# Kernel optimization log

Hardware: AMD Instinct MI355X
Metric: run time of the kernel (lower is better)

Reference implementation:

```python
import jax, jax.numpy as jnp
import numpy as np

B, S, D = 2, 2048, 2048
H = 16
KV_RANK = 512
NOPE, ROPE = 128, 64
QK_HD = NOPE + ROPE  # 192
V_HD = 128
SCALE = QK_HD ** -0.5
EPS = 1.1920929e-07  # torch RMSNorm default eps = finfo(fp32).eps
NEG = -1e9


def rmsnorm(x, w):
    return x * jax.lax.rsqrt(jnp.mean(x * x, axis=-1, keepdims=True) + EPS) * w


def apply_rope(x, freqs):
    # x: (b, s, h, r) interleaved pairs; freqs: (s, r//2) angles
    sh = x.shape
    xr = x.reshape(*sh[:-1], -1, 2)
    a, b = xr[..., 0], xr[..., 1]
    cos = jnp.cos(freqs)[None, :, None, :]
    sin = jnp.sin(freqs)[None, :, None, :]
    return jnp.stack([a * cos - b * sin, a * sin + b * cos], axis=-1).reshape(sh)


def setup_inputs() -> dict:
    key = jax.random.key(0)
    ks = jax.random.split(key, 8)
    inv = lambda k, shape, fan_in: jax.random.uniform(k, shape, jnp.float32, -1.0, 1.0) / np.sqrt(fan_in)
    x = jax.random.normal(ks[0], (B, S, D), jnp.float32)
    freqs = jax.random.uniform(ks[1], (S, ROPE // 2), jnp.float32) * np.float32(np.pi)
    mask = jnp.where(jnp.triu(jnp.ones((S, S), bool), k=1), jnp.float32(NEG), jnp.float32(0.0))
    wq_w = inv(ks[2], (H * QK_HD, D), D)
    wq_b = jnp.zeros((H * QK_HD,), jnp.float32)
    wkv_a_w = inv(ks[3], (KV_RANK + ROPE, D), D)
    wkv_a_b = jnp.zeros((KV_RANK + ROPE,), jnp.float32)
    kv_norm_w = jnp.ones((KV_RANK,), jnp.float32)
    wkv_b_w = inv(ks[4], (H * (NOPE + V_HD), KV_RANK), KV_RANK)
    wo_w = inv(ks[5], (D, H * V_HD), H * V_HD)
    wo_b = jnp.zeros((D,), jnp.float32)
    return dict(x=x, freqs=freqs, mask=mask, wq_w=wq_w, wq_b=wq_b,
                wkv_a_w=wkv_a_w, wkv_a_b=wkv_a_b, kv_norm_w=kv_norm_w,
                wkv_b_w=wkv_b_w, wo_w=wo_w, wo_b=wo_b)


def reference(x, freqs, mask, wq_w, wq_b, wkv_a_w, wkv_a_b, kv_norm_w, wkv_b_w, wo_w, wo_b):
    b, s, _ = x.shape
    # q projection (q_lora_rank == 0 path)
    q = (x @ wq_w.T + wq_b).reshape(b, s, H, QK_HD)
    q_nope, q_pe = q[..., :NOPE], q[..., NOPE:]
    q_pe = apply_rope(q_pe, freqs)
    # latent kv projection
    kv = x @ wkv_a_w.T + wkv_a_b
    kv, k_pe = kv[..., :KV_RANK], kv[..., KV_RANK:]
    k_pe = apply_rope(k_pe[:, :, None, :], freqs)[:, :, 0, :]  # (b, t, r)
    kv_proj = rmsnorm(kv, kv_norm_w)  # (b, t, c)
    wkv_b = wkv_b_w.reshape(H, NOPE + V_HD, KV_RANK)
    # absorb K-nope projection into q
    q_nope = jnp.einsum('bshd,hdc->bshc', q_nope, wkv_b[:, :NOPE])
    scores = (jnp.einsum('bshc,btc->bsht', q_nope, kv_proj)
              + jnp.einsum('bshr,btr->bsht', q_pe, k_pe)) * SCALE
    scores = scores + mask[None, :, None, :]
    scores = jax.nn.softmax(scores.astype(jnp.float32), axis=-1).astype(x.dtype)
    out = jnp.einsum('bsht,btc->bshc', scores, kv_proj)
    out = jnp.einsum('bshc,hdc->bshd', out, wkv_b[:, -V_HD:])
    return out.reshape(b, s, H * V_HD) @ wo_w.T + wo_b
```

## Files before the change

### kernel.cpp

```cpp
#include <hip/hip_runtime.h>
#include <hip/hip_bf16.h>
#include <math.h>

#define B_ 2
#define S_ 2048
#define H_ 16
#define SCALE_ 0.07216878364870323f
#define SL2_ (0.07216878364870323f * 1.4426950408889634f)
#define EPS_ 1.1920929e-07f
#define M0_ 8.0f

typedef __attribute__((ext_vector_type(8))) short bf16x8;
typedef __attribute__((ext_vector_type(4))) float f32x4;
union U4 { uint4 u; bf16x8 v; f32x4 f; };

__device__ __forceinline__ uint bfbits(float x) {
    uint u = __float_as_uint(x);
    return (u + 0x7fffu + ((u >> 16) & 1u)) >> 16;
}
__device__ __forceinline__ uint pack2bf(float a, float b) {
    return bfbits(a) | (bfbits(b) << 16);
}
__device__ __forceinline__ uint cvtpk(float a, float b) {
    uint r;
    asm("v_cvt_pk_bf16_f32 %0, %1, %2" : "=v"(r) : "v"(a), "v"(b));
    return r;
}
__device__ __forceinline__ void gld_lds16(const ushort* g, ushort* l) {
    __builtin_amdgcn_global_load_lds(
        (const __attribute__((address_space(1))) uint*)g,
        (__attribute__((address_space(3))) uint*)l, 16, 0, 0);
}

template<bool OUT_BF16>
__global__ __launch_bounds__(256) void mgemm(
    const ushort* __restrict__ A, int lda, long long aOff1, long long aOff2,
    const ushort* __restrict__ Bm, int ldb, long long bOff1, long long bOff2,
    const float* __restrict__ bias, float scale,
    void* __restrict__ Cv, int ldc, long long cOff1, long long cOff2,
    int K, int zDiv)
{
    __shared__ ushort As[128 * 32];
    __shared__ ushort Bs[128 * 32];

    const int z = blockIdx.z;
    const int z1 = z % zDiv, z2 = z / zDiv;
    A  += z1 * aOff1 + z2 * aOff2;
    Bm += z1 * bOff1 + z2 * bOff2;
    const long long cBase = z1 * cOff1 + z2 * cOff2;

    const int n0 = blockIdx.x * 128;
    const int m0 = blockIdx.y * 128;
    const int tid = threadIdx.x;
    const int w   = tid >> 6;
    const int l   = tid & 63;
    const int m   = l & 15;
    const int q4  = l >> 4;
    const int mw  = (w & 1) * 64;
    const int nw  = (w >> 1) * 64;
    const int sr  = l >> 2;
    const int sc  = l & 3;

    f32x4 acc[4][4];
#pragma unroll
    for (int i = 0; i < 4; ++i)
#pragma unroll
        for (int j = 0; j < 4; ++j) acc[i][j] = (f32x4){0.f, 0.f, 0.f, 0.f};

    for (int k0 = 0; k0 < K; k0 += 32) {
#pragma unroll
        for (int jj = 0; jj < 2; ++jj) {
            const int slot = w * 2 + jj;
            const int row  = slot * 16 + sr;
            const int g    = sc ^ ((row >> 1) & 3);
            gld_lds16(&A[(long long)(m0 + row) * lda + k0 + g * 8], &As[slot * 512]);
            gld_lds16(&Bm[(long long)(n0 + row) * ldb + k0 + g * 8], &Bs[slot * 512]);
        }
        __syncthreads();

        U4 af[4], bf[4];
#pragma unroll
        for (int i = 0; i < 4; ++i) {
            const int ra = mw + i * 16 + m;
            af[i].u = *(const uint4*)&As[ra * 32 + (q4 ^ ((ra >> 1) & 3)) * 8];
            const int rb = nw + i * 16 + m;
            bf[i].u = *(const uint4*)&Bs[rb * 32 + (q4 ^ ((rb >> 1) & 3)) * 8];
        }
#pragma unroll
        for (int i = 0; i < 4; ++i)
#pragma unroll
            for (int j = 0; j < 4; ++j)
                acc[i][j] = __builtin_amdgcn_mfma_f32_16x16x32_bf16(
                    af[i].v, bf[j].v, acc[i][j], 0, 0, 0);
        __syncthreads();
    }

#pragma unroll
    for (int j = 0; j < 4; ++j) {
        const int cn = n0 + nw + j * 16 + m;
        const float bv = bias ? bias[cn] : 0.0f;
#pragma unroll
        for (int i = 0; i < 4; ++i) {
            const int rw = m0 + mw + i * 16 + q4 * 4;
#pragma unroll
            for (int r = 0; r < 4; ++r) {
                const float val = acc[i][j][r] * scale + bv;
                if (OUT_BF16)
                    ((ushort*)Cv)[cBase + (long long)(rw + r) * ldc + cn] =
                        (ushort)bfbits(val);
                else
                    ((float*)Cv)[cBase + (long long)(rw + r) * ldc + cn] = val;
            }
        }
    }
}

__global__ __launch_bounds__(256) void conv_all(
    const float* __restrict__ x, const float* __restrict__ wq,
    const float* __restrict__ wkva, const float* __restrict__ wo,
    const float* __restrict__ wkvb,
    ushort* __restrict__ x_bf, ushort* __restrict__ wq_bf,
    ushort* __restrict__ wkva_bf, ushort* __restrict__ wo_bf,
    ushort* __restrict__ wkvbK, ushort* __restrict__ wkvbV)
{
    const int bid = blockIdx.x;
    const int tid = threadIdx.x;
    if (bid < 8192) {
        const long long i = ((long long)bid * 256 + tid) * 4;
        float4 v = *(const float4*)&x[i];
        uint2 p; p.x = pack2bf(v.x, v.y); p.y = pack2bf(v.z, v.w);
        *(uint2*)&x_bf[i] = p;
    } else if (bid < 14336) {
        const long long i = ((long long)(bid - 8192) * 256 + tid) * 4;
        float4 v = *(const float4*)&wq[i];
        uint2 p; p.x = pack2bf(v.x, v.y); p.y = pack2bf(v.z, v.w);
        *(uint2*)&wq_bf[i] = p;
    } else if (bid < 15616) {
        const int i = ((bid - 14336) * 256 + tid) * 4;
        const int r = i >> 11;
        uint2 p = make_uint2(0u, 0u);
        if (r < 576) {
            float4 v = *(const float4*)&wkva[i];
            p.x = pack2bf(v.x, v.y); p.y = pack2bf(v.z, v.w);
        }
        *(uint2*)&wkva_bf[i] = p;
    } else if (bid < 19712) {
        const long long i = ((long long)(bid - 15616) * 256 + tid) * 4;
        float4 v = *(const float4*)&wo[i];
        uint2 p; p.x = pack2bf(v.x, v.y); p.y = pack2bf(v.z, v.w);
        *(uint2*)&wo_bf[i] = p;
    } else if (bid < 20736) {
        const int i = ((bid - 19712) * 256 + tid) * 4;
        const int h = i >> 16, rem = i & 65535;
        float4 v = *(const float4*)&wkvb[((long long)(h * 256)) * 512 + rem];
        uint2 p; p.x = pack2bf(v.x, v.y); p.y = pack2bf(v.z, v.w);
        *(uint2*)&wkvbK[i] = p;
    } else {
        const int i = ((bid - 20736) * 256 + tid) * 4;
        const int h = i >> 16, rem = i & 65535;
        float4 v = *(const float4*)&wkvb[((long long)(h * 256 + 128)) * 512 + rem];
        uint2 p; p.x = pack2bf(v.x, v.y); p.y = pack2bf(v.z, v.w);
        *(uint2*)&wkvbV[i] = p;
    }
}

__global__ __launch_bounds__(256) void qprep(
    const float* __restrict__ q_raw, const float* __restrict__ freqs,
    ushort* __restrict__ q192)
{
    const int idx = blockIdx.x * 256 + threadIdx.x;
    const int row = idx / 48;
    const int c4  = idx % 48;
    const int bs = row >> 4, h = row & 15;
    const float* src = q_raw + (long long)bs * 3072 + h * 192;
    if (c4 < 32) {
        const int d = c4 * 4;
        float4 v = *(const float4*)&src[d];
        uint2 p;
        p.x = pack2bf(v.x * SL2_, v.y * SL2_);
        p.y = pack2bf(v.z * SL2_, v.w * SL2_);
        *(uint2*)&q192[(long long)row * 192 + d] = p;
    } else {
        const int j = c4 - 32;
        const int s = bs & 2047;
        const float f0 = freqs[s * 32 + j * 2];
        const float f1 = freqs[s * 32 + j * 2 + 1];
        float c0, s0, c1, s1;
        __sincosf(f0, &s0, &c0);
        __sincosf(f1, &s1, &c1);
        float4 v = *(const float4*)&src[128 + j * 4];
        uint2 p;
        p.x = pack2bf((v.x * c0 - v.y * s0) * SL2_, (v.x * s0 + v.y * c0) * SL2_);
        p.y = pack2bf((v.z * c1 - v.w * s1) * SL2_, (v.z * s1 + v.w * c1) * SL2_);
        *(uint2*)&q192[(long long)row * 192 + 128 + j * 4] = p;
    }
}

__global__ __launch_bounds__(64) void kv_post_kernel(
    const float* __restrict__ kv_raw, const float* __restrict__ bias,
    const float* __restrict__ w, const float* __restrict__ freqs,
    ushort* __restrict__ kv_h)
{
    const int bs = blockIdx.x;
    const int lane = threadIdx.x;
    const float* src = kv_raw + (long long)bs * 640;
    ushort* dst = kv_h + (long long)bs * 576;

    const int c = 4 * lane;
    float4 v0 = *(const float4*)&src[c];
    float4 v1 = *(const float4*)&src[256 + c];
    float4 b0 = *(const float4*)&bias[c];
    float4 b1 = *(const float4*)&bias[256 + c];
    v0.x += b0.x; v0.y += b0.y; v0.z += b0.z; v0.w += b0.w;
    v1.x += b1.x; v1.y += b1.y; v1.z += b1.z; v1.w += b1.w;
    float ss = v0.x * v0.x + v0.y * v0.y + v0.z * v0.z + v0.w * v0.w +
               v1.x * v1.x + v1.y * v1.y + v1.z * v1.z + v1.w * v1.w;
#pragma unroll
    for (int o = 32; o; o >>= 1) ss += __shfl_xor(ss, o, 64);
    const float rs = rsqrtf(ss * (1.0f / 512.0f) + EPS_);

    float4 w0 = *(const float4*)&w[c];
    float4 w1 = *(const float4*)&w[256 + c];
    uint2 p0, p1;
    p0.x = pack2bf(v0.x * rs * w0.x, v0.y * rs * w0.y);
    p0.y = pack2bf(v0.z * rs * w0.z, v0.w * rs * w0.w);
    p1.x = pack2bf(v1.x * rs * w1.x, v1.y * rs * w1.y);
    p1.y = pack2bf(v1.z * rs * w1.z, v1.w * rs * w1.w);
    *(uint2*)&dst[c] = p0;
    *(uint2*)&dst[256 + c] = p1;

    if (lane < 32) {
        const int s = bs & 2047;
        const float f = freqs[s * 32 + lane];
        float cs, sn;
        __sincosf(f, &sn, &cs);
        const float a  = src[512 + 2 * lane]     + bias[512 + 2 * lane];
        const float b2 = src[512 + 2 * lane + 1] + bias[512 + 2 * lane + 1];
        *(uint*)&dst[512 + 2 * lane] = pack2bf(a * cs - b2 * sn, a * sn + b2 * cs);
    }
}

__global__ __launch_bounds__(256) void prep_all(
    const ushort* __restrict__ K_h, const ushort* __restrict__ V_hT,
    const ushort* __restrict__ kv_h,
    uint4* __restrict__ khimg, uint4* __restrict__ vhimg,
    uint4* __restrict__ rimg)
{
    const int bid = blockIdx.x;
    if (bid < 4096) {
        const int g = bid * 256 + threadIdx.x;
        const int lane = g & 63, ck = (g >> 6) & 7, h = (g >> 9) & 15;
        const int tile = (g >> 13) & 63, b = g >> 19;
        const int m = lane & 15, q4 = lane >> 4, f = ck >> 1, s = ck & 1;
        const uint4 v = *(const uint4*)&K_h[
            ((long long)(b * S_ + tile * 32 + s * 16 + m)) * 2048 + h * 128 + f * 32 + q4 * 8];
        khimg[(((long long)(b * 64 + tile) * 16 + h) * 8 + ck) * 64 + lane] = v;
    } else if (bid < 8192) {
        const int g = (bid - 4096) * 256 + threadIdx.x;
        const int lane = g & 63, c = (g >> 6) & 7, h = (g >> 9) & 15;
        const int tile = (g >> 13) & 63, b = g >> 19;
        const int m = lane & 15, q4 = lane >> 4;
        const uint4 v = *(const uint4*)&V_hT[
            ((long long)((b * 16 + h) * 128 + c * 16 + m)) * 2048 + tile * 32 + q4 * 8];
        vhimg[(((long long)(b * 64 + tile) * 16 + h) * 8 + c) * 64 + lane] = v;
    } else {
        const int g = (bid - 8192) * 256 + threadIdx.x;
        const int lane = g & 63, ck = (g >> 6) & 3, tile = (g >> 8) & 63, b = g >> 14;
        const int m = lane & 15, q4 = lane >> 4, f2 = ck >> 1, s = ck & 1;
        const uint4 v = *(const uint4*)&kv_h[
            ((long long)(b * S_ + tile * 32 + s * 16 + m)) * 576 + 512 + f2 * 32 + q4 * 8];
        rimg[((long long)(b * 64 + tile) * 4 + ck) * 64 + lane] = v;
    }
}

__global__ __launch_bounds__(256, 2) void attn_kernel(
    const ushort* __restrict__ q192,
    const uint4*  __restrict__ khimg,
    const uint4*  __restrict__ rimg,
    const uint4*  __restrict__ vhimg,
    float* __restrict__ part_o,
    float* __restrict__ part_l)
{
    __shared__ uint buf[2][20 * 256];

    const int p    = blockIdx.x;
    const int h    = blockIdx.y;
    const int zz   = blockIdx.z;
    const int b    = zz >> 1;
    const int par  = zz & 1;
    const int tid  = threadIdx.x;
    const int wid  = tid >> 6;
    const int lane = tid & 63;
    const int m    = lane & 15;
    const int q4   = lane >> 4;
    const bool odd = q4 & 1;

    auto stage = [&](int bs, int it) {
        const long long tb = (long long)(b * 64 + it);
        const uint4* kb = khimg + ((tb * 16 + h) * 8) * 64;
        const uint4* rb = rimg  + (tb * 4) * 64;
        const uint4* vb = vhimg + ((tb * 16 + h) * 8) * 64;
        ushort* l = (ushort*)&buf[bs][0];
        gld_lds16((const ushort*)(kb + (wid    ) * 64 + lane), l + (wid     ) * 512);
        gld_lds16((const ushort*)(kb + (wid + 4) * 64 + lane), l + (wid +  4) * 512);
        gld_lds16((const ushort*)(rb + (wid    ) * 64 + lane), l + (wid +  8) * 512);
        gld_lds16((const ushort*)(vb + (wid    ) * 64 + lane), l + (wid + 12) * 512);
        gld_lds16((const ushort*)(vb + (wid + 4) * 64 + lane), l + (wid + 16) * 512);
    };

    int cur = 0;
    for (int pass = 0; pass < 2; ++pass) {
        const int chunk = pass ? p : (15 - p);
        const int row0a = chunk * 128 + wid * 16;
        const int row0b = row0a + 64;
        const int sRa   = row0a + m;
        const int sRb   = row0b + m;

        U4 qfa[6], qfb[6];
        {
            const uint4* qpa = (const uint4*)(q192 + ((long long)(b * S_ + sRa) * H_ + h) * 192);
            const uint4* qpb = (const uint4*)(q192 + ((long long)(b * S_ + sRb) * H_ + h) * 192);
#pragma unroll
            for (int f = 0; f < 6; ++f) { qfa[f].u = qpa[f * 4 + q4]; qfb[f].u = qpb[f * 4 + q4]; }
        }

        f32x4 oA[8], oB[8];
#pragma unroll
        for (int c = 0; c < 8; ++c) {
            oA[c] = (f32x4){0.f, 0.f, 0.f, 0.f};
            oB[c] = (f32x4){0.f, 0.f, 0.f, 0.f};
        }
        float lA = 0.0f, lB = 0.0f;

        auto softpack = [&](const f32x4 s0, const f32x4 s1, int t0v, int rw0,
                            float& lac) -> U4 {
            float p00, p01, p02, p03, p10, p11, p12, p13;
            if (t0v + 31 <= rw0) {
                p00 = exp2f(s0[0] - M0_); p01 = exp2f(s0[1] - M0_);
                p02 = exp2f(s0[2] - M0_); p03 = exp2f(s0[3] - M0_);
                p10 = exp2f(s1[0] - M0_); p11 = exp2f(s1[1] - M0_);
                p12 = exp2f(s1[2] - M0_); p13 = exp2f(s1[3] - M0_);
            } else {
                const int sR = rw0 + m;
                const int tb0 = t0v + q4 * 4;
                const int tb1 = tb0 + 16;
                p00 = (tb0 + 0 <= sR) ? exp2f(s0[0] - M0_) : 0.0f;
                p01 = (tb0 + 1 <= sR) ? exp2f(s0[1] - M0_) : 0.0f;
                p02 = (tb0 + 2 <= sR) ? exp2f(s0[2] - M0_) : 0.0f;
                p03 = (tb0 + 3 <= sR) ? exp2f(s0[3] - M0_) : 0.0f;
                p10 = (tb1 + 0 <= sR) ? exp2f(s1[0] - M0_) : 0.0f;
                p11 = (tb1 + 1 <= sR) ? exp2f(s1[1] - M0_) : 0.0f;
                p12 = (tb1 + 2 <= sR) ? exp2f(s1[2] - M0_) : 0.0f;
                p13 = (tb1 + 3 <= sR) ? exp2f(s1[3] - M0_) : 0.0f;
            }
            lac += (p00 + p01) + (p02 + p03) + (p10 + p11) + (p12 + p13);
            uint X0 = cvtpk(p00, p01), X1 = cvtpk(p02, p03);
            uint Y0 = cvtpk(p10, p11), Y1 = cvtpk(p12, p13);
            asm("v_permlane32_swap_b32 %0, %1" : "+v"(X0), "+v"(Y0));
            asm("v_permlane32_swap_b32 %0, %1" : "+v"(X1), "+v"(Y1));
            uint u0 = odd ? X0 : Y0;
            uint u1 = odd ? X1 : Y1;
            uint w0 = (uint)__builtin_amdgcn_ds_swizzle((int)u0, 0x401F);
            uint w1 = (uint)__builtin_amdgcn_ds_swizzle((int)u1, 0x401F);
            U4 bb;
            bb.u.x = odd ? w0 : X0;
            bb.u.y = odd ? w1 : X1;
            bb.u.z = odd ? Y0 : w0;
            bb.u.w = odd ? Y1 : w1;
            return bb;
        };

        const int nT2 = 2 * chunk + 2;
        __syncthreads();
        stage(cur, par);

        for (int v = 0; v < nT2; ++v) {
            const int it = 2 * v + par;
            const int t0 = it * 32;
            __syncthreads();
            if (v + 1 < nT2) stage(cur ^ 1, it + 2);
            __builtin_amdgcn_sched_barrier(0);

            const uint* bb0 = &buf[cur][0];
            const int abase = lane * 4;
            const bool liveB = (t0 <= row0b + 15);
            const bool liveA = (t0 <= row0a + 15);
            const bool twoA  = (t0 < row0a);
            const bool twoB  = (t0 < row0b);

            if (liveB) {
                f32x4 sA0 = (f32x4){0.f,0.f,0.f,0.f}, sA1 = (f32x4){0.f,0.f,0.f,0.f};
                f32x4 sB0 = (f32x4){0.f,0.f,0.f,0.f}, sB1 = (f32x4){0.f,0.f,0.f,0.f};

                if (twoA) {
#pragma unroll
                    for (int f = 0; f < 6; ++f) {
                        const int ck = (f < 4) ? f * 2 : (f - 4) * 2 + 8;
                        U4 a0, a1;
                        a0.u = *(const uint4*)&bb0[ck * 256 + abase];
                        a1.u = *(const uint4*)&bb0[(ck + 1) * 256 + abase];
                        sA0 = __builtin_amdgcn_mfma_f32_16x16x32_bf16(a0.v, qfa[f].v, sA0, 0, 0, 0);
                        sB0 = __builtin_amdgcn_mfma_f32_16x16x32_bf16(a0.v, qfb[f].v, sB0, 0, 0, 0);
                        sA1 = __builtin_amdgcn_mfma_f32_16x16x32_bf16(a1.v, qfa[f].v, sA1, 0, 0, 0);
                        sB1 = __builtin_amdgcn_mfma_f32_16x16x32_bf16(a1.v, qfb[f].v, sB1, 0, 0, 0);
                    }
                } else {
#pragma unroll
                    for (int f = 0; f < 6; ++f) {
                        const int ck = (f < 4) ? f * 2 : (f - 4) * 2 + 8;
                        U4 a0;
                        a0.u = *(const uint4*)&bb0[ck * 256 + abase];
                        if (liveA)
                            sA0 = __builtin_amdgcn_mfma_f32_16x16x32_bf16(a0.v, qfa[f].v, sA0, 0, 0, 0);
                        sB0 = __builtin_amdgcn_mfma_f32_16x16x32_bf16(a0.v, qfb[f].v, sB0, 0, 0, 0);
                        if (twoB) {
                            U4 a1;
                            a1.u = *(const uint4*)&bb0[(ck + 1) * 256 + abase];
                            sB1 = __builtin_amdgcn_mfma_f32_16x16x32_bf16(a1.v, qfb[f].v, sB1, 0, 0, 0);
                        }
                    }
                }

                U4 bbB = softpack(sB0, sB1, t0, row0b, lB);
                if (liveA) {
                    U4 bbA = softpack(sA0, sA1, t0, row0a, lA);
#pragma unroll
                    for (int c = 0; c < 8; ++c) {
                        U4 av; av.u = *(const uint4*)&bb0[(12 + c) * 256 + abase];
                        oB[c] = __builtin_amdgcn_mfma_f32_16x16x32_bf16(av.v, bbB.v, oB[c], 0, 0, 0);
                        oA[c] = __builtin_amdgcn_mfma_f32_16x16x32_bf16(av.v, bbA.v, oA[c], 0, 0, 0);
                    }
                } else {
#pragma unroll
                    for (int c = 0; c < 8; ++c) {
                        U4 av; av.u = *(const uint4*)&bb0[(12 + c) * 256 + abase];
                        oB[c] = __builtin_amdgcn_mfma_f32_16x16x32_bf16(av.v, bbB.v, oB[c], 0, 0, 0);
                    }
                }
            }
            cur ^= 1;
        }

        lA += __shfl_xor(lA, 16, 64);
        lA += __shfl_xor(lA, 32, 64);
        lB += __shfl_xor(lB, 16, 64);
        lB += __shfl_xor(lB, 32, 64);

        const int cid  = (b * 16 + h) * 16 + chunk;
        const int slot = cid * 2 + par;
        float* po = part_o + (long long)slot * 16384;
        const int rA = wid * 16 + m;
        const int rB = rA + 64;
#pragma unroll
        for (int c = 0; c < 8; ++c) {
            *(f32x4*)&po[rA * 128 + c * 16 + q4 * 4] = oA[c];
            *(f32x4*)&po[rB * 128 + c * 16 + q4 * 4] = oB[c];
        }
        if (q4 == 0) {
            part_l[slot * 128 + rA] = lA;
            part_l[slot * 128 + rB] = lB;
        }
    }
}

__global__ __launch_bounds__(256) void combine_kernel(
    const float* __restrict__ part_o, const float* __restrict__ part_l,
    ushort* __restrict__ o_h)
{
    const int idx = blockIdx.x * 256 + threadIdx.x;
    const int d4  = (idx & 31) * 4;
    const int r   = (idx >> 5) & 127;
    const int cid = idx >> 12;
    const int chunk = cid & 15, h = (cid >> 4) & 15, b = cid >> 8;
    const long long s0 = (long long)(cid * 2) * 16384 + r * 128 + d4;
    float4 a = *(const float4*)&part_o[s0];
    float4 c = *(const float4*)&part_o[s0 + 16384];
    const float l = part_l[cid * 256 + r] + part_l[cid * 256 + 128 + r];
    const float inv = 1.0f / l;
    uint2 pk;
    pk.x = cvtpk((a.x + c.x) * inv, (a.y + c.y) * inv);
    pk.y = cvtpk((a.z + c.z) * inv, (a.w + c.w) * inv);
    const int s = chunk * 128 + r;
    *(uint2*)&o_h[(((long long)(b * S_ + s)) * H_ + h) * 128 + d4] = pk;
}

extern "C" void kernel_launch(void* const* d_in, const int* in_sizes, int n_in,
                              void* d_out, int out_size, void* d_ws, size_t ws_size,
                              hipStream_t stream)
{
    const float* x         = (const float*)d_in[0];
    const float* freqs     = (const float*)d_in[1];
    const float* wq_w      = (const float*)d_in[3];
    const float* wq_b      = (const float*)d_in[4];
    const float* wkv_a_w   = (const float*)d_in[5];
    const float* wkv_a_b   = (const float*)d_in[6];
    const float* kv_norm_w = (const float*)d_in[7];
    const float* wkv_b_w   = (const float*)d_in[8];
    const float* wo_w      = (const float*)d_in[9];
    const float* wo_b      = (const float*)d_in[10];
    float* out = (float*)d_out;

    char* w = (char*)d_ws;
    ushort* wo_bf   = (ushort*)w;  w += 8388608;
    uint4*  khimg   = (uint4*)w;   w += 16777216;
    uint4*  vhimg   = (uint4*)w;   w += 16777216;
    uint4*  rimg    = (uint4*)w;   w += 524288;
    ushort* q192    = (ushort*)w;  w += 25165824;
    ushort* o_h     = (ushort*)w;  w += 16777216;
    char* SCR = w;
    ushort* x_bf    = (ushort*)(SCR);
    ushort* wq_bf   = (ushort*)(SCR + 16777216);
    ushort* wkva_bf = (ushort*)(SCR + 29360128);
    ushort* wkvbK   = (ushort*)(SCR + 31981568);
    ushort* wkvbV   = (ushort*)(SCR + 34078720);
    float*  kv_raw  = (float*)(SCR + 36175872);
    float*  q_raw   = (float*)(SCR + 46661632);
    ushort* kv_h    = (ushort*)(SCR);
    ushort* K_h     = (ushort*)(SCR + 4718592);
    ushort* V_hT    = (ushort*)(SCR + 36175872);
    float*  part_o  = (float*)(SCR);
    float*  part_l  = (float*)(SCR + 67108864);

    dim3 blk(256);

    conv_all<<<dim3(21760), blk, 0, stream>>>(
        x, wq_w, wkv_a_w, wo_w, wkv_b_w,
        x_bf, wq_bf, wkva_bf, wo_bf, wkvbK, wkvbV);

    mgemm<false><<<dim3(24, 32, 1), blk, 0, stream>>>(
        x_bf, 2048, 0LL, 0LL, wq_bf, 2048, 0LL, 0LL, wq_b, 1.0f,
        q_raw, 3072, 0LL, 0LL, 2048, 1);

    mgemm<false><<<dim3(5, 32, 1), blk, 0, stream>>>(
        x_bf, 2048, 0LL, 0LL, wkva_bf, 2048, 0LL, 0LL, nullptr, 1.0f,
        kv_raw, 640, 0LL, 0LL, 2048, 1);

    qprep<<<dim3(12288), blk, 0, stream>>>(q_raw, freqs, q192);

    kv_post_kernel<<<dim3(4096), dim3(64), 0, stream>>>(
        kv_raw, wkv_a_b, kv_norm_w, freqs, kv_h);

    mgemm<true><<<dim3(1, 16, 32), blk, 0, stream>>>(
        kv_h, 576, 0LL, (long long)S_ * 576,
        wkvbK, 512, 65536LL, 0LL, nullptr, 1.0f,
        K_h, 2048, 128LL, (long long)S_ * 2048, 512, 16);
    mgemm<true><<<dim3(16, 1, 32), blk, 0, stream>>>(
        wkvbV, 512, 65536LL, 0LL,
        kv_h, 576, 0LL, (long long)S_ * 576, nullptr, 1.0f,
        V_hT, 2048, 262144LL, 4194304LL, 512, 16);

    prep_all<<<dim3(8320), blk, 0, stream>>>(K_h, V_hT, kv_h, khimg, vhimg, rimg);

    attn_kernel<<<dim3(8, 16, 4), blk, 0, stream>>>(
        q192, khimg, rimg, vhimg, part_o, part_l);

    combine_kernel<<<dim3(8192), blk, 0, stream>>>(part_o, part_l, o_h);

    mgemm<false><<<dim3(16, 32, 1), blk, 0, stream>>>(
        o_h, 2048, 0LL, 0LL, wo_bf, 2048, 0LL, 0LL, wo_b, 1.0f,
        out, 2048, 0LL, 0LL, 2048, 1);
}
```

Baseline: 466.0 us.

## Write attention tile images directly from GEMM epilogues and drop prep_all

The K and V projection GEMMs now scatter their bf16 results straight into the tiled khimg/vhimg layouts the attention kernel consumes. kv_post writes the rope part directly into rimg, which removes the separate prep_all repacking kernel and its intermediate K_h/V_hT buffers. The GEMM block index is also remapped so neighbouring blocks spread across groups of 8, aimed at cache or XCD locality. The attention grid is reordered so heads and batch sit in the fastest-varying dimension. The scattered 2-byte epilogue stores may coalesce poorly.

```diff
diff --git a/kernel.cpp b/kernel.cpp
--- a/kernel.cpp
+++ b/kernel.cpp
@@ -32,7 +32,7 @@
         (__attribute__((address_space(3))) uint*)l, 16, 0, 0);
 }
 
-template<bool OUT_BF16>
+template<int OM>
 __global__ __launch_bounds__(256) void mgemm(
     const ushort* __restrict__ A, int lda, long long aOff1, long long aOff2,
     const ushort* __restrict__ Bm, int ldb, long long bOff1, long long bOff2,
@@ -49,8 +49,19 @@
     Bm += z1 * bOff1 + z2 * bOff2;
     const long long cBase = z1 * cOff1 + z2 * cOff2;
 
-    const int n0 = blockIdx.x * 128;
-    const int m0 = blockIdx.y * 128;
+    int bx = blockIdx.x, by = blockIdx.y;
+    {
+        const int gx = gridDim.x, total = gx * gridDim.y;
+        if ((total & 7) == 0) {
+            const int flat = bx + gx * by;
+            const int nx = total >> 3;
+            const int flat2 = (flat & 7) * nx + (flat >> 3);
+            bx = flat2 % gx;
+            by = flat2 / gx;
+        }
+    }
+    const int n0 = bx * 128;
+    const int m0 = by * 128;
     const int tid = threadIdx.x;
     const int w   = tid >> 6;
     const int l   = tid & 63;
@@ -105,11 +116,23 @@
 #pragma unroll
             for (int r = 0; r < 4; ++r) {
                 const float val = acc[i][j][r] * scale + bv;
-                if (OUT_BF16)
-                    ((ushort*)Cv)[cBase + (long long)(rw + r) * ldc + cn] =
-                        (ushort)bfbits(val);
-                else
+                if (OM == 0) {
                     ((float*)Cv)[cBase + (long long)(rw + r) * ldc + cn] = val;
+                } else if (OM == 2) {
+                    const int t = rw + r, d = cn;
+                    const long long idx =
+                        ((((long long)(z2 * 64 + (t >> 5)) * 16 + z1) * 8
+                          + (d >> 5) * 2 + ((t >> 4) & 1)) * 64
+                         + ((d >> 3) & 3) * 16 + (t & 15)) * 8 + (d & 7);
+                    ((ushort*)Cv)[idx] = (ushort)bfbits(val);
+                } else {
+                    const int d = rw + r, t = cn;
+                    const long long idx =
+                        ((((long long)(z2 * 64 + (t >> 5)) * 16 + z1) * 8
+                          + (d >> 4)) * 64
+                         + ((t >> 3) & 3) * 16 + (d & 15)) * 8 + (t & 7);
+                    ((ushort*)Cv)[idx] = (ushort)bfbits(val);
+                }
             }
         }
     }
@@ -199,7 +222,7 @@
 __global__ __launch_bounds__(64) void kv_post_kernel(
     const float* __restrict__ kv_raw, const float* __restrict__ bias,
     const float* __restrict__ w, const float* __restrict__ freqs,
-    ushort* __restrict__ kv_h)
+    ushort* __restrict__ kv_h, uint* __restrict__ rimg)
 {
     const int bs = blockIdx.x;
     const int lane = threadIdx.x;
@@ -230,46 +253,18 @@
     *(uint2*)&dst[256 + c] = p1;
 
     if (lane < 32) {
-        const int s = bs & 2047;
-        const float f = freqs[s * 32 + lane];
+        const int b = bs >> 11, s = bs & 2047;
+        const int j = lane;
+        const float f = freqs[s * 32 + j];
         float cs, sn;
         __sincosf(f, &sn, &cs);
-        const float a  = src[512 + 2 * lane]     + bias[512 + 2 * lane];
-        const float b2 = src[512 + 2 * lane + 1] + bias[512 + 2 * lane + 1];
-        *(uint*)&dst[512 + 2 * lane] = pack2bf(a * cs - b2 * sn, a * sn + b2 * cs);
-    }
-}
-
-__global__ __launch_bounds__(256) void prep_all(
-    const ushort* __restrict__ K_h, const ushort* __restrict__ V_hT,
-    const ushort* __restrict__ kv_h,
-    uint4* __restrict__ khimg, uint4* __restrict__ vhimg,
-    uint4* __restrict__ rimg)
-{
-    const int bid = blockIdx.x;
-    if (bid < 4096) {
-        const int g = bid * 256 + threadIdx.x;
-        const int lane = g & 63, ck = (g >> 6) & 7, h = (g >> 9) & 15;
-        const int tile = (g >> 13) & 63, b = g >> 19;
-        const int m = lane & 15, q4 = lane >> 4, f = ck >> 1, s = ck & 1;
-        const uint4 v = *(const uint4*)&K_h[
-            ((long long)(b * S_ + tile * 32 + s * 16 + m)) * 2048 + h * 128 + f * 32 + q4 * 8];
-        khimg[(((long long)(b * 64 + tile) * 16 + h) * 8 + ck) * 64 + lane] = v;
-    } else if (bid < 8192) {
-        const int g = (bid - 4096) * 256 + threadIdx.x;
-        const int lane = g & 63, c = (g >> 6) & 7, h = (g >> 9) & 15;
-        const int tile = (g >> 13) & 63, b = g >> 19;
-        const int m = lane & 15, q4 = lane >> 4;
-        const uint4 v = *(const uint4*)&V_hT[
-            ((long long)((b * 16 + h) * 128 + c * 16 + m)) * 2048 + tile * 32 + q4 * 8];
-        vhimg[(((long long)(b * 64 + tile) * 16 + h) * 8 + c) * 64 + lane] = v;
-    } else {
-        const int g = (bid - 8192) * 256 + threadIdx.x;
-        const int lane = g & 63, ck = (g >> 6) & 3, tile = (g >> 8) & 63, b = g >> 14;
-        const int m = lane & 15, q4 = lane >> 4, f2 = ck >> 1, s = ck & 1;
-        const uint4 v = *(const uint4*)&kv_h[
-            ((long long)(b * S_ + tile * 32 + s * 16 + m)) * 576 + 512 + f2 * 32 + q4 * 8];
-        rimg[((long long)(b * 64 + tile) * 4 + ck) * 64 + lane] = v;
+        const float a  = src[512 + 2 * j]     + bias[512 + 2 * j];
+        const float b2 = src[512 + 2 * j + 1] + bias[512 + 2 * j + 1];
+        const uint p = pack2bf(a * cs - b2 * sn, a * sn + b2 * cs);
+        const long long idx =
+            (((long long)(b * 64 + (s >> 5)) * 4 + (j >> 4) * 2 + ((s >> 4) & 1)) * 64
+             + ((j >> 2) & 3) * 16 + (s & 15)) * 4 + (j & 3);
+        rimg[idx] = p;
     }
 }
 
@@ -283,11 +278,11 @@
 {
     __shared__ uint buf[2][20 * 256];
 
-    const int p    = blockIdx.x;
-    const int h    = blockIdx.y;
-    const int zz   = blockIdx.z;
-    const int b    = zz >> 1;
-    const int par  = zz & 1;
+    const int hb   = blockIdx.x;
+    const int h    = hb & 15;
+    const int b    = hb >> 4;
+    const int p    = blockIdx.y;
+    const int par  = blockIdx.z;
     const int tid  = threadIdx.x;
     const int wid  = tid >> 6;
     const int lane = tid & 63;
@@ -516,8 +511,6 @@
     float*  kv_raw  = (float*)(SCR + 36175872);
     float*  q_raw   = (float*)(SCR + 46661632);
     ushort* kv_h    = (ushort*)(SCR);
-    ushort* K_h     = (ushort*)(SCR + 4718592);
-    ushort* V_hT    = (ushort*)(SCR + 36175872);
     float*  part_o  = (float*)(SCR);
     float*  part_l  = (float*)(SCR + 67108864);
 
@@ -527,36 +520,34 @@
         x, wq_w, wkv_a_w, wo_w, wkv_b_w,
         x_bf, wq_bf, wkva_bf, wo_bf, wkvbK, wkvbV);
 
-    mgemm<false><<<dim3(24, 32, 1), blk, 0, stream>>>(
+    mgemm<0><<<dim3(24, 32, 1), blk, 0, stream>>>(
         x_bf, 2048, 0LL, 0LL, wq_bf, 2048, 0LL, 0LL, wq_b, 1.0f,
         q_raw, 3072, 0LL, 0LL, 2048, 1);
 
-    mgemm<false><<<dim3(5, 32, 1), blk, 0, stream>>>(
+    mgemm<0><<<dim3(5, 32, 1), blk, 0, stream>>>(
         x_bf, 2048, 0LL, 0LL, wkva_bf, 2048, 0LL, 0LL, nullptr, 1.0f,
         kv_raw, 640, 0LL, 0LL, 2048, 1);
 
     qprep<<<dim3(12288), blk, 0, stream>>>(q_raw, freqs, q192);
 
     kv_post_kernel<<<dim3(4096), dim3(64), 0, stream>>>(
-        kv_raw, wkv_a_b, kv_norm_w, freqs, kv_h);
-
-    mgemm<true><<<dim3(1, 16, 32), blk, 0, stream>>>(
+        kv_raw, wkv_a_b, kv_norm_w, freqs, kv_h, (uint*)rimg);
+
+    mgemm<2><<<dim3(1, 16, 32), blk, 0, stream>>>(
         kv_h, 576, 0LL, (long long)S_ * 576,
         wkvbK, 512, 65536LL, 0LL, nullptr, 1.0f,
-        K_h, 2048, 128LL, (long long)S_ * 2048, 512, 16);
-    mgemm<true><<<dim3(16, 1, 32), blk, 0, stream>>>(
+        khimg, 0, 0LL, 0LL, 512, 16);
+    mgemm<3><<<dim3(16, 1, 32), blk, 0, stream>>>(
         wkvbV, 512, 65536LL, 0LL,
         kv_h, 576, 0LL, (long long)S_ * 576, nullptr, 1.0f,
-        V_hT, 2048, 262144LL, 4194304LL, 512, 16);
-
-    prep_all<<<dim3(8320), blk, 0, stream>>>(K_h, V_hT, kv_h, khimg, vhimg, rimg);
-
-    attn_kernel<<<dim3(8, 16, 4), blk, 0, stream>>>(
+        vhimg, 0, 0LL, 0LL, 512, 16);
+
+    attn_kernel<<<dim3(32, 8, 2), blk, 0, stream>>>(
         q192, khimg, rimg, vhimg, part_o, part_l);
 
     combine_kernel<<<dim3(8192), blk, 0, stream>>>(part_o, part_l, o_h);
 
-    mgemm<false><<<dim3(16, 32, 1), blk, 0, stream>>>(
+    mgemm<0><<<dim3(16, 32, 1), blk, 0, stream>>>(
         o_h, 2048, 0LL, 0LL, wo_bf, 2048, 0LL, 0LL, wo_b, 1.0f,
         out, 2048, 0LL, 0LL, 2048, 1);
 }
```

Result: faster. 443.6 us (-4.8%).
